# Performance work log

Hardware: AMD Instinct MI355X
Metric: run time of the kernel (lower is better)

## Reference

```python
import jax, jax.numpy as jnp
import numpy as np

T, N, E, D, NL = 2, 4096, 4096, 128, 2  # types, nodes, hyperedges, in_dim, num_layers
DENSITY = 0.002  # ~8 hyperedges per node


def setup_inputs() -> dict:
    key = jax.random.key(0)
    k1, k2, k3, k4 = jax.random.split(key, 4)
    x = jax.random.normal(k1, (N, D), dtype=jnp.float32)
    # binary incidence matrices, one per hyperedge type
    H = (jax.random.uniform(k2, (T, N, E)) < DENSITY).astype(jnp.float32)
    # nn.Linear weights (torch convention: [out, in]) and biases, per layer per type
    W = jax.random.normal(k3, (NL, T, D, D), dtype=jnp.float32) * (1.0 / np.sqrt(D))
    b = jax.random.normal(k4, (NL, T, D), dtype=jnp.float32) * 0.05
    return {"x": x, "H": H, "W": W, "b": b}


def reference(x, H, W, b):
    # degree normalizations (set_matrices): D_v^{-1/2}, D_e^{-1}, zeros kept at zero
    dV = H.sum(-1)                                  # [T,N]
    dVis = jnp.where(dV > 0, dV ** -0.5, 0.0)       # [T,N]
    dE = H.sum(1)                                   # [T,E]
    dEinv = jnp.where(dE > 0, 1.0 / dE, 0.0)        # [T,E]

    node_out = [x]
    review_out = []
    num_layers = W.shape[0]
    for l in range(num_layers):
        # per-type Linear: y = x @ W_k.T + b_k (dropout p=0 -> identity)
        xw = jnp.einsum('nd,tod->tno', x, W[l]) + b[l][:, None, :]   # [T,N,D]
        # e = L @ xw with L = Dv^{-1/2} H De^{-1} H^T Dv^{-1/2}
        y = dVis[..., None] * xw                                     # [T,N,D]
        ye = dEinv[..., None] * jnp.einsum('tne,tnd->ted', H, y)     # [T,E,D]
        e = dVis[..., None] * jnp.einsum('tne,ted->tnd', H, ye)      # [T,N,D]
        e = jax.nn.leaky_relu(e, 0.01)                               # non_linear
        # o = O @ e = De^{-1} H^T e; aggregator='sum' over types
        o = (dEinv[..., None] * jnp.einsum('tne,tnd->ted', H, e)).sum(0)  # [E,D]
        x = e.sum(0)                                                 # [N,D]
        node_out.append(x)
        review_out.append(o)

    return (jnp.stack(node_out).mean(0), jnp.stack(review_out).mean(0))
```

## Files before the change

### kernel.cpp

```cpp
#include <hip/hip_runtime.h>

#define T_ 2
#define N_ 4096
#define E_ 4096
#define D_ 128
#define CAP 64
#define PAD 16
#define SENT 8192
#define UPR 64

__device__ __forceinline__ unsigned f2bf_rne(float f) {
    unsigned u = __float_as_uint(f);
    return (u + 0x7FFFu + ((u >> 16) & 1u)) >> 16;
}
__device__ __forceinline__ unsigned pack2(float lo, float hi) {
    return f2bf_rne(lo) | (f2bf_rne(hi) << 16);
}

__device__ __forceinline__ float2 gather64(const unsigned* __restrict__ src,
        const int* __restrict__ row, int c, int lane) {
    const int4* r4 = (const int4*)row;
    int4 i0 = r4[0], i1 = r4[1], i2 = r4[2], i3 = r4[3];
    float sx = 0.f, sy = 0.f;
#define G1(id) { unsigned v = src[(size_t)(id) * UPR + lane]; \
                 sx += __uint_as_float(v << 16); \
                 sy += __uint_as_float(v & 0xFFFF0000u); }
    G1(i0.x) G1(i0.y) G1(i0.z) G1(i0.w)
    G1(i1.x) G1(i1.y) G1(i1.z) G1(i1.w)
    G1(i2.x) G1(i2.y) G1(i2.z) G1(i2.w)
    G1(i3.x) G1(i3.y) G1(i3.z) G1(i3.w)
    for (int j = PAD; j < c; ++j) G1(row[j])
#undef G1
    float2 r = {sx, sy};
    return r;
}

__device__ __forceinline__ float2 gather64w(const unsigned* __restrict__ src,
        const float* __restrict__ wgt, const int* __restrict__ row, int c, int lane) {
    const int4* r4 = (const int4*)row;
    int4 i0 = r4[0], i1 = r4[1], i2 = r4[2], i3 = r4[3];
    float sx = 0.f, sy = 0.f;
#define G1(id) { unsigned v = src[(size_t)(id) * UPR + lane]; float w = wgt[id]; \
                 sx += w * __uint_as_float(v << 16); \
                 sy += w * __uint_as_float(v & 0xFFFF0000u); }
    G1(i0.x) G1(i0.y) G1(i0.z) G1(i0.w)
    G1(i1.x) G1(i1.y) G1(i1.z) G1(i1.w)
    G1(i2.x) G1(i2.y) G1(i2.z) G1(i2.w)
    G1(i3.x) G1(i3.y) G1(i3.z) G1(i3.w)
    for (int j = PAD; j < c; ++j) G1(row[j])
#undef G1
    float2 r = {sx, sy};
    return r;
}

__device__ __forceinline__ void xw_tile(int slot, int l,
        const float* __restrict__ xsrc, const float* __restrict__ W,
        const float* __restrict__ b, uint2* __restrict__ y2,
        float* s_xs, float* s_ws) {
    int t = slot >> 7;
    int nb = (slot >> 1) & 63, ob = slot & 1;
    int n0 = nb * 64, o0 = ob * 64;
    int tid = threadIdx.x;
    int tx = tid & 15, ty = tid >> 4;
    const float* Wg = W + ((size_t)(l * T_ + t) * D_ + o0) * D_;
    const float* xg = xsrc + (size_t)n0 * D_;
    float acc[4][4] = {};
    for (int kc = 0; kc < 4; ++kc) {
        __syncthreads();
        for (int i = tid; i < 512; i += 256) {
            int r = i >> 3, k4 = i & 7;
            *(float4*)(s_xs + r * 36 + k4 * 4) =
                *(const float4*)(xg + (size_t)r * D_ + kc * 32 + k4 * 4);
            int k4s = k4 ^ ((r >> 2) & 7);
            *(float4*)(s_ws + r * 32 + k4s * 4) =
                *(const float4*)(Wg + (size_t)r * D_ + kc * 32 + k4 * 4);
        }
        __syncthreads();
        #pragma unroll
        for (int k4 = 0; k4 < 8; ++k4) {
            float4 xv[4], wv[4];
            #pragma unroll
            for (int rr = 0; rr < 4; ++rr)
                xv[rr] = *(const float4*)(s_xs + (ty * 4 + rr) * 36 + k4 * 4);
            int k4s = k4 ^ (tx & 7);
            #pragma unroll
            for (int cc = 0; cc < 4; ++cc)
                wv[cc] = *(const float4*)(s_ws + (tx * 4 + cc) * 32 + k4s * 4);
            #pragma unroll
            for (int rr = 0; rr < 4; ++rr)
                #pragma unroll
                for (int cc = 0; cc < 4; ++cc)
                    acc[rr][cc] += xv[rr].x * wv[cc].x + xv[rr].y * wv[cc].y
                                 + xv[rr].z * wv[cc].z + xv[rr].w * wv[cc].w;
        }
    }
    const float* bg = b + (size_t)(l * T_ + t) * D_;
    float4 bv = *(const float4*)(bg + o0 + tx * 4);
    #pragma unroll
    for (int rr = 0; rr < 4; ++rr) {
        int n = n0 + ty * 4 + rr;
        uint2 ov;
        ov.x = pack2(acc[rr][0] + bv.x, acc[rr][1] + bv.y);
        ov.y = pack2(acc[rr][2] + bv.z, acc[rr][3] + bv.w);
        y2[(size_t)(t * N_ + n) * (UPR / 2) + (o0 >> 2) + tx] = ov;
    }
}

__global__ __launch_bounds__(256) void k_scan_xw0(const float* __restrict__ H,
        float* __restrict__ dVis, int* __restrict__ cntNE,
        int* __restrict__ adjNE, int* __restrict__ cntENp,
        int* __restrict__ adjEN,
        const float* __restrict__ x, const float* __restrict__ W,
        const float* __restrict__ b, uint2* __restrict__ y2,
        unsigned* __restrict__ y2u, unsigned* __restrict__ ye2u,
        unsigned* __restrict__ e2u) {
    __shared__ float s_xs[64 * 36];
    __shared__ float s_ws[64 * 32];
    int bid = blockIdx.x;
    if (bid >= 2048) {
        xw_tile(bid - 2048, 0, x, W, b, y2, s_xs, s_ws);
        return;
    }
    int row = bid * 4 + (threadIdx.x >> 6);
    int lane = threadIdx.x & 63;
    int t = row >> 12;
    if (lane < PAD) adjEN[(size_t)row * CAP + lane] = SENT;
    else if (lane == PAD) cntENp[row * 16] = 0;
    if (bid == 0 && threadIdx.x < 64) {
        y2u[(size_t)SENT * UPR + threadIdx.x] = 0u;
        ye2u[(size_t)SENT * UPR + threadIdx.x] = 0u;
        e2u[(size_t)SENT * UPR + threadIdx.x] = 0u;
        if (threadIdx.x == 0) dVis[SENT] = 0.0f;
    }
    const float4* row4 = (const float4*)(H + (size_t)row * E_);
    unsigned long long mask = 0;
    #pragma unroll
    for (int i = 0; i < 16; ++i) {
        float4 v = row4[i * 64 + lane];
        unsigned mm = 0;
        if (v.x != 0.0f) mm |= 1u;
        if (v.y != 0.0f) mm |= 2u;
        if (v.z != 0.0f) mm |= 4u;
        if (v.w != 0.0f) mm |= 8u;
        mask |= (unsigned long long)mm << (i * 4);
    }
    int cnt = __popcll(mask);
    int incl = cnt;
    #pragma unroll
    for (int off = 1; off < 64; off <<= 1) {
        int u = __shfl_up(incl, off);
        if (lane >= off) incl += u;
    }
    int pos = incl - cnt;
    int total = __shfl(incl, 63);
    int* adjrow = adjNE + (size_t)row * CAP;
    unsigned long long m = mask;
    while (m) {
        int bpos = __builtin_ctzll(m);
        m &= m - 1;
        int e = ((bpos >> 2) << 8) + lane * 4 + (bpos & 3);
        if (pos < CAP) adjrow[pos] = t * E_ + e;
        ++pos;
    }
    if (lane < PAD - total) adjrow[total + lane] = SENT;
    if (lane == 63) {
        cntNE[row] = total < CAP ? total : CAP;
        dVis[row] = total > 0 ? rsqrtf((float)total) : 0.0f;
    }
}

__global__ __launch_bounds__(256) void k_inv(const int* __restrict__ cntNE,
        const int* __restrict__ adjNE, int* __restrict__ cntENp,
        int* __restrict__ adjEN) {
    int row = blockIdx.x * 4 + (threadIdx.x >> 6);
    int lane = threadIdx.x & 63;
    int c = cntNE[row];
    if (lane < c) {
        int eg = adjNE[(size_t)row * CAP + lane];
        int slot = atomicAdd(&cntENp[eg * 16], 1);
        if (slot < CAP) adjEN[(size_t)eg * CAP + slot] = row;
    }
}

__global__ __launch_bounds__(256) void k_ye_w(const unsigned* __restrict__ y2u,
        const float* __restrict__ dVis, const int* __restrict__ cntENp,
        const int* __restrict__ adjEN, unsigned* __restrict__ ye2u) {
    int u = threadIdx.x >> 6, lane = threadIdx.x & 63;
    int vr = blockIdx.x * 4 + u;
    int c = cntENp[vr * 16];
    if (c > CAP) c = CAP;
    float dE = c > 0 ? 1.0f / (float)c : 0.0f;
    float2 g = gather64w(y2u, dVis, adjEN + (size_t)vr * CAP, c, lane);
    ye2u[(size_t)vr * UPR + lane] = pack2(dE * g.x, dE * g.y);
}

__device__ __forceinline__ void o_unit(int e, int u, int lane,
        const unsigned* __restrict__ e2u, const int* __restrict__ cntENp,
        const int* __restrict__ adjEN, float2* __restrict__ revacc2,
        float2* __restrict__ outrev2, int last, float2 (*sb)[64]) {
    int t = u & 1;
    int r = t * E_ + e;
    int c = cntENp[r * 16];
    if (c > CAP) c = CAP;
    float dE = c > 0 ? 1.0f / (float)c : 0.0f;
    float2 g = gather64(e2u, adjEN + (size_t)r * CAP, c, lane);
    float2 a = {dE * g.x, dE * g.y};
    sb[u][lane] = a;
    __syncthreads();
    if (t == 0) {
        float2 o2 = sb[u | 1][lane];
        float2 tot = {a.x + o2.x, a.y + o2.y};
        size_t i = (size_t)e * UPR + lane;
        if (!last) revacc2[i] = tot;
        else {
            float2 ra = revacc2[i];
            float2 o = {(ra.x + tot.x) * 0.5f, (ra.y + tot.y) * 0.5f};
            outrev2[i] = o;
        }
    }
}

__global__ __launch_bounds__(256) void k_e(const unsigned* __restrict__ ye2u,
        const float* __restrict__ dVis, const int* __restrict__ cntNE,
        const int* __restrict__ adjNE, unsigned* __restrict__ e2u,
        const float* __restrict__ x0, float* __restrict__ xsum0,
        float* __restrict__ outnode, int last) {
    __shared__ float2 sb[4][64];
    int u = threadIdx.x >> 6, lane = threadIdx.x & 63;
    int t = u & 1;
    int n = blockIdx.x * 2 + (u >> 1);
    int r = t * N_ + n;
    int c = cntNE[r];
    float2 g = gather64(ye2u, adjNE + (size_t)r * CAP, c, lane);
    float dv = dVis[r];
    float e0 = dv * g.x; e0 = e0 >= 0.f ? e0 : 0.01f * e0;
    float e1 = dv * g.y; e1 = e1 >= 0.f ? e1 : 0.01f * e1;
    e2u[(size_t)r * UPR + lane] = pack2(e0, e1);
    float2 mine = {e0, e1};
    sb[u][lane] = mine;
    __syncthreads();
    if (t == 0) {
        float2 o2 = sb[u | 1][lane];
        float2 xnew = {e0 + o2.x, e1 + o2.y};
        size_t i = (size_t)n * UPR + lane;
        if (!last) ((float2*)xsum0)[i] = xnew;
        else {
            float2 xv = ((const float2*)x0)[i];
            float2 xs = ((const float2*)xsum0)[i];
            float2 o = {(xv.x + xs.x + xnew.x) * (1.0f / 3.0f),
                        (xv.y + xs.y + xnew.y) * (1.0f / 3.0f)};
            ((float2*)outnode)[i] = o;
        }
    }
}

__global__ __launch_bounds__(256) void k_xw1_o0(const float* __restrict__ xsum0,
        const float* __restrict__ W, const float* __restrict__ b,
        uint2* __restrict__ y2,
        const unsigned* __restrict__ e2u, const int* __restrict__ cntENp,
        const int* __restrict__ adjEN, float* __restrict__ revacc) {
    __shared__ float s_xs[64 * 36];
    __shared__ float s_ws[64 * 32];
    __shared__ float2 sb[4][64];
    int bid = blockIdx.x;
    if (bid < 256) {
        xw_tile(bid, 1, xsum0, W, b, y2, s_xs, s_ws);
    } else {
        int u = threadIdx.x >> 6, lane = threadIdx.x & 63;
        int e = (bid - 256) * 2 + (u >> 1);
        o_unit(e, u, lane, e2u, cntENp, adjEN, (float2*)revacc, nullptr, 0, sb);
    }
}

__global__ __launch_bounds__(256) void k_o(const unsigned* __restrict__ e2u,
        const int* __restrict__ cntENp, const int* __restrict__ adjEN,
        float* __restrict__ revacc, float* __restrict__ outrev) {
    __shared__ float2 sb[4][64];
    int u = threadIdx.x >> 6, lane = threadIdx.x & 63;
    int e = blockIdx.x * 2 + (u >> 1);
    o_unit(e, u, lane, e2u, cntENp, adjEN, (float2*)revacc, (float2*)outrev, 1, sb);
}

extern "C" void kernel_launch(void* const* d_in, const int* in_sizes, int n_in,
                              void* d_out, int out_size, void* d_ws, size_t ws_size,
                              hipStream_t stream) {
    const float* x = (const float*)d_in[0];
    const float* H = (const float*)d_in[1];
    const float* W = (const float*)d_in[2];
    const float* b = (const float*)d_in[3];
    float* outnode = (float*)d_out;
    float* outrev  = (float*)d_out + (size_t)N_ * D_;

    char* p = (char*)d_ws;
    auto alloc = [&](size_t bytes) {
        char* r = p;
        p += (bytes + 255) & ~(size_t)255;
        return r;
    };
    float*    dVis   = (float*)alloc(((size_t)T_ * N_ + 1) * 4);
    int*      cntNE  = (int*)  alloc((size_t)T_ * N_ * 4);
    int*      cntENp = (int*)  alloc((size_t)T_ * E_ * 16 * 4);
    int*      adjNE  = (int*)  alloc((size_t)T_ * N_ * CAP * 4);
    int*      adjEN  = (int*)  alloc((size_t)T_ * E_ * CAP * 4);
    unsigned* y2u    = (unsigned*)alloc((size_t)(SENT + 1) * UPR * 4);
    unsigned* ye2u   = (unsigned*)alloc((size_t)(SENT + 1) * UPR * 4);
    unsigned* e2u    = (unsigned*)alloc((size_t)(SENT + 1) * UPR * 4);
    float*    xsum0  = (float*)alloc((size_t)N_ * D_ * 4);
    float*    revacc = (float*)alloc((size_t)E_ * D_ * 4);

    k_scan_xw0<<<2048 + 256, 256, 0, stream>>>(H, dVis, cntNE, adjNE, cntENp,
            adjEN, x, W, b, (uint2*)y2u, y2u, ye2u, e2u);
    k_inv<<<2048, 256, 0, stream>>>(cntNE, adjNE, cntENp, adjEN);
    k_ye_w<<<2048, 256, 0, stream>>>(y2u, dVis, cntENp, adjEN, ye2u);
    k_e<<<2048, 256, 0, stream>>>(ye2u, dVis, cntNE, adjNE, e2u, x, xsum0,
                                  outnode, 0);
    k_xw1_o0<<<256 + 2048, 256, 0, stream>>>(xsum0, W, b, (uint2*)y2u,
            e2u, cntENp, adjEN, revacc);
    k_ye_w<<<2048, 256, 0, stream>>>(y2u, dVis, cntENp, adjEN, ye2u);
    k_e<<<2048, 256, 0, stream>>>(ye2u, dVis, cntNE, adjNE, e2u, x, xsum0,
                                  outnode, 1);
    k_o<<<2048, 256, 0, stream>>>(e2u, cntENp, adjEN, revacc, outrev);
}
```

Measured before the change: 86.08 us.

## Fuse hyperedge aggregation into node gather via two-hop traversal with packed weights

Removes the k_ye_w kernel and its ye2u intermediate. Each node now gathers directly over its hyperedges and then over each hyperedge's member nodes, recomputing the hyperedge sums on the fly. The node degree weight is quantised to 16 bits and packed beside the node index in the edge-to-node adjacency list, which removes a separate dVis lookup per neighbour. This saves two launches and a round trip through memory, but each hyperedge sum is recomputed once per member node, roughly eight times the gather traffic, and the 16-bit weight quantisation adds rounding error.

```diff
diff --git a/kernel.cpp b/kernel.cpp
--- a/kernel.cpp
+++ b/kernel.cpp
@@ -8,6 +8,7 @@
 #define PAD 16
 #define SENT 8192
 #define UPR 64
+#define W16S 65535.0f
 
 __device__ __forceinline__ unsigned f2bf_rne(float f) {
     unsigned u = __float_as_uint(f);
@@ -17,14 +18,14 @@
     return f2bf_rne(lo) | (f2bf_rne(hi) << 16);
 }
 
-__device__ __forceinline__ float2 gather64(const unsigned* __restrict__ src,
-        const int* __restrict__ row, int c, int lane) {
-    const int4* r4 = (const int4*)row;
-    int4 i0 = r4[0], i1 = r4[1], i2 = r4[2], i3 = r4[3];
+__device__ __forceinline__ float2 gather16_id(const unsigned* __restrict__ src,
+        const unsigned* __restrict__ row, int c, int lane) {
+    const uint4* r4 = (const uint4*)row;
+    uint4 i0 = r4[0], i1 = r4[1], i2 = r4[2], i3 = r4[3];
     float sx = 0.f, sy = 0.f;
-#define G1(id) { unsigned v = src[(size_t)(id) * UPR + lane]; \
-                 sx += __uint_as_float(v << 16); \
-                 sy += __uint_as_float(v & 0xFFFF0000u); }
+#define G1(w) { unsigned v = src[(size_t)((w) & 0xFFFFu) * UPR + lane]; \
+                sx += __uint_as_float(v << 16); \
+                sy += __uint_as_float(v & 0xFFFF0000u); }
     G1(i0.x) G1(i0.y) G1(i0.z) G1(i0.w)
     G1(i1.x) G1(i1.y) G1(i1.z) G1(i1.w)
     G1(i2.x) G1(i2.y) G1(i2.z) G1(i2.w)
@@ -35,21 +36,27 @@
     return r;
 }
 
-__device__ __forceinline__ float2 gather64w(const unsigned* __restrict__ src,
-        const float* __restrict__ wgt, const int* __restrict__ row, int c, int lane) {
-    const int4* r4 = (const int4*)row;
-    int4 i0 = r4[0], i1 = r4[1], i2 = r4[2], i3 = r4[3];
+__device__ __forceinline__ float2 inner16(int eg, int lane,
+        const unsigned* __restrict__ y2u, const int* __restrict__ cntENp,
+        const unsigned* __restrict__ adjEN) {
+    int cE = cntENp[eg * 16];
+    if (cE > CAP) cE = CAP;
+    float dE = cE > 0 ? 1.0f / (float)cE : 0.0f;
+    const unsigned* en = adjEN + (size_t)eg * CAP;
+    const uint4* r4 = (const uint4*)en;
+    uint4 i0 = r4[0], i1 = r4[1], i2 = r4[2], i3 = r4[3];
     float sx = 0.f, sy = 0.f;
-#define G1(id) { unsigned v = src[(size_t)(id) * UPR + lane]; float w = wgt[id]; \
-                 sx += w * __uint_as_float(v << 16); \
-                 sy += w * __uint_as_float(v & 0xFFFF0000u); }
+#define G1(w) { unsigned v = y2u[(size_t)((w) & 0xFFFFu) * UPR + lane]; \
+                float wt = (float)((w) >> 16) * (1.0f / W16S); \
+                sx += wt * __uint_as_float(v << 16); \
+                sy += wt * __uint_as_float(v & 0xFFFF0000u); }
     G1(i0.x) G1(i0.y) G1(i0.z) G1(i0.w)
     G1(i1.x) G1(i1.y) G1(i1.z) G1(i1.w)
     G1(i2.x) G1(i2.y) G1(i2.z) G1(i2.w)
     G1(i3.x) G1(i3.y) G1(i3.z) G1(i3.w)
-    for (int j = PAD; j < c; ++j) G1(row[j])
+    for (int j = PAD; j < cE; ++j) G1(en[j])
 #undef G1
-    float2 r = {sx, sy};
+    float2 r = {dE * sx, dE * sy};
     return r;
 }
 
@@ -109,11 +116,10 @@
 __global__ __launch_bounds__(256) void k_scan_xw0(const float* __restrict__ H,
         float* __restrict__ dVis, int* __restrict__ cntNE,
         int* __restrict__ adjNE, int* __restrict__ cntENp,
-        int* __restrict__ adjEN,
+        unsigned* __restrict__ adjEN,
         const float* __restrict__ x, const float* __restrict__ W,
         const float* __restrict__ b, uint2* __restrict__ y2,
-        unsigned* __restrict__ y2u, unsigned* __restrict__ ye2u,
-        unsigned* __restrict__ e2u) {
+        unsigned* __restrict__ y2u, unsigned* __restrict__ e2u) {
     __shared__ float s_xs[64 * 36];
     __shared__ float s_ws[64 * 32];
     int bid = blockIdx.x;
@@ -128,8 +134,9 @@
     else if (lane == PAD) cntENp[row * 16] = 0;
     if (bid == 0 && threadIdx.x < 64) {
         y2u[(size_t)SENT * UPR + threadIdx.x] = 0u;
-        ye2u[(size_t)SENT * UPR + threadIdx.x] = 0u;
         e2u[(size_t)SENT * UPR + threadIdx.x] = 0u;
+        if (threadIdx.x < PAD) adjEN[(size_t)SENT * CAP + threadIdx.x] = SENT;
+        if (threadIdx.x == PAD) cntENp[SENT * 16] = 0;
         if (threadIdx.x == 0) dVis[SENT] = 0.0f;
     }
     const float4* row4 = (const float4*)(H + (size_t)row * E_);
@@ -170,59 +177,24 @@
 }
 
 __global__ __launch_bounds__(256) void k_inv(const int* __restrict__ cntNE,
-        const int* __restrict__ adjNE, int* __restrict__ cntENp,
-        int* __restrict__ adjEN) {
+        const int* __restrict__ adjNE, const float* __restrict__ dVis,
+        int* __restrict__ cntENp, unsigned* __restrict__ adjEN) {
     int row = blockIdx.x * 4 + (threadIdx.x >> 6);
     int lane = threadIdx.x & 63;
     int c = cntNE[row];
     if (lane < c) {
         int eg = adjNE[(size_t)row * CAP + lane];
+        unsigned w16 = (unsigned)(dVis[row] * W16S + 0.5f);
         int slot = atomicAdd(&cntENp[eg * 16], 1);
-        if (slot < CAP) adjEN[(size_t)eg * CAP + slot] = row;
-    }
-}
-
-__global__ __launch_bounds__(256) void k_ye_w(const unsigned* __restrict__ y2u,
-        const float* __restrict__ dVis, const int* __restrict__ cntENp,
-        const int* __restrict__ adjEN, unsigned* __restrict__ ye2u) {
-    int u = threadIdx.x >> 6, lane = threadIdx.x & 63;
-    int vr = blockIdx.x * 4 + u;
-    int c = cntENp[vr * 16];
-    if (c > CAP) c = CAP;
-    float dE = c > 0 ? 1.0f / (float)c : 0.0f;
-    float2 g = gather64w(y2u, dVis, adjEN + (size_t)vr * CAP, c, lane);
-    ye2u[(size_t)vr * UPR + lane] = pack2(dE * g.x, dE * g.y);
-}
-
-__device__ __forceinline__ void o_unit(int e, int u, int lane,
-        const unsigned* __restrict__ e2u, const int* __restrict__ cntENp,
-        const int* __restrict__ adjEN, float2* __restrict__ revacc2,
-        float2* __restrict__ outrev2, int last, float2 (*sb)[64]) {
-    int t = u & 1;
-    int r = t * E_ + e;
-    int c = cntENp[r * 16];
-    if (c > CAP) c = CAP;
-    float dE = c > 0 ? 1.0f / (float)c : 0.0f;
-    float2 g = gather64(e2u, adjEN + (size_t)r * CAP, c, lane);
-    float2 a = {dE * g.x, dE * g.y};
-    sb[u][lane] = a;
-    __syncthreads();
-    if (t == 0) {
-        float2 o2 = sb[u | 1][lane];
-        float2 tot = {a.x + o2.x, a.y + o2.y};
-        size_t i = (size_t)e * UPR + lane;
-        if (!last) revacc2[i] = tot;
-        else {
-            float2 ra = revacc2[i];
-            float2 o = {(ra.x + tot.x) * 0.5f, (ra.y + tot.y) * 0.5f};
-            outrev2[i] = o;
-        }
-    }
-}
-
-__global__ __launch_bounds__(256) void k_e(const unsigned* __restrict__ ye2u,
+        if (slot < CAP)
+            adjEN[(size_t)eg * CAP + slot] = (unsigned)row | (w16 << 16);
+    }
+}
+
+__global__ __launch_bounds__(256) void k_e2hop(const unsigned* __restrict__ y2u,
         const float* __restrict__ dVis, const int* __restrict__ cntNE,
-        const int* __restrict__ adjNE, unsigned* __restrict__ e2u,
+        const int* __restrict__ adjNE, const int* __restrict__ cntENp,
+        const unsigned* __restrict__ adjEN, unsigned* __restrict__ e2u,
         const float* __restrict__ x0, float* __restrict__ xsum0,
         float* __restrict__ outnode, int last) {
     __shared__ float2 sb[4][64];
@@ -230,11 +202,29 @@
     int t = u & 1;
     int n = blockIdx.x * 2 + (u >> 1);
     int r = t * N_ + n;
-    int c = cntNE[r];
-    float2 g = gather64(ye2u, adjNE + (size_t)r * CAP, c, lane);
+    int cn = cntNE[r];
+    const int* an = adjNE + (size_t)r * CAP;
+    const int4* a4 = (const int4*)an;
+    float sx = 0.f, sy = 0.f;
+#define EG4(v) { \
+        float2 p0 = inner16(v.x, lane, y2u, cntENp, adjEN); \
+        float2 p1 = inner16(v.y, lane, y2u, cntENp, adjEN); \
+        float2 p2 = inner16(v.z, lane, y2u, cntENp, adjEN); \
+        float2 p3 = inner16(v.w, lane, y2u, cntENp, adjEN); \
+        sx += (p0.x + p1.x) + (p2.x + p3.x); \
+        sy += (p0.y + p1.y) + (p2.y + p3.y); }
+    if (cn > 0)  { int4 v = a4[0]; EG4(v) }
+    if (cn > 4)  { int4 v = a4[1]; EG4(v) }
+    if (cn > 8)  { int4 v = a4[2]; EG4(v) }
+    if (cn > 12) { int4 v = a4[3]; EG4(v) }
+#undef EG4
+    for (int j = PAD; j < cn; ++j) {
+        float2 p = inner16(an[j], lane, y2u, cntENp, adjEN);
+        sx += p.x; sy += p.y;
+    }
     float dv = dVis[r];
-    float e0 = dv * g.x; e0 = e0 >= 0.f ? e0 : 0.01f * e0;
-    float e1 = dv * g.y; e1 = e1 >= 0.f ? e1 : 0.01f * e1;
+    float e0 = dv * sx; e0 = e0 >= 0.f ? e0 : 0.01f * e0;
+    float e1 = dv * sy; e1 = e1 >= 0.f ? e1 : 0.01f * e1;
     e2u[(size_t)r * UPR + lane] = pack2(e0, e1);
     float2 mine = {e0, e1};
     sb[u][lane] = mine;
@@ -254,11 +244,37 @@
     }
 }
 
+__device__ __forceinline__ void o_unit(int e, int u, int lane,
+        const unsigned* __restrict__ e2u, const int* __restrict__ cntENp,
+        const unsigned* __restrict__ adjEN, float2* __restrict__ revacc2,
+        float2* __restrict__ outrev2, int last, float2 (*sb)[64]) {
+    int t = u & 1;
+    int r = t * E_ + e;
+    int c = cntENp[r * 16];
+    if (c > CAP) c = CAP;
+    float dE = c > 0 ? 1.0f / (float)c : 0.0f;
+    float2 g = gather16_id(e2u, adjEN + (size_t)r * CAP, c, lane);
+    float2 a = {dE * g.x, dE * g.y};
+    sb[u][lane] = a;
+    __syncthreads();
+    if (t == 0) {
+        float2 o2 = sb[u | 1][lane];
+        float2 tot = {a.x + o2.x, a.y + o2.y};
+        size_t i = (size_t)e * UPR + lane;
+        if (!last) revacc2[i] = tot;
+        else {
+            float2 ra = revacc2[i];
+            float2 o = {(ra.x + tot.x) * 0.5f, (ra.y + tot.y) * 0.5f};
+            outrev2[i] = o;
+        }
+    }
+}
+
 __global__ __launch_bounds__(256) void k_xw1_o0(const float* __restrict__ xsum0,
         const float* __restrict__ W, const float* __restrict__ b,
         uint2* __restrict__ y2,
         const unsigned* __restrict__ e2u, const int* __restrict__ cntENp,
-        const int* __restrict__ adjEN, float* __restrict__ revacc) {
+        const unsigned* __restrict__ adjEN, float* __restrict__ revacc) {
     __shared__ float s_xs[64 * 36];
     __shared__ float s_ws[64 * 32];
     __shared__ float2 sb[4][64];
@@ -273,7 +289,7 @@
 }
 
 __global__ __launch_bounds__(256) void k_o(const unsigned* __restrict__ e2u,
-        const int* __restrict__ cntENp, const int* __restrict__ adjEN,
+        const int* __restrict__ cntENp, const unsigned* __restrict__ adjEN,
         float* __restrict__ revacc, float* __restrict__ outrev) {
     __shared__ float2 sb[4][64];
     int u = threadIdx.x >> 6, lane = threadIdx.x & 63;
@@ -299,25 +315,22 @@
     };
     float*    dVis   = (float*)alloc(((size_t)T_ * N_ + 1) * 4);
     int*      cntNE  = (int*)  alloc((size_t)T_ * N_ * 4);
-    int*      cntENp = (int*)  alloc((size_t)T_ * E_ * 16 * 4);
+    int*      cntENp = (int*)  alloc(((size_t)T_ * E_ * 16 + 16) * 4);
     int*      adjNE  = (int*)  alloc((size_t)T_ * N_ * CAP * 4);
-    int*      adjEN  = (int*)  alloc((size_t)T_ * E_ * CAP * 4);
+    unsigned* adjEN  = (unsigned*)alloc(((size_t)T_ * E_ + 1) * CAP * 4);
     unsigned* y2u    = (unsigned*)alloc((size_t)(SENT + 1) * UPR * 4);
-    unsigned* ye2u   = (unsigned*)alloc((size_t)(SENT + 1) * UPR * 4);
     unsigned* e2u    = (unsigned*)alloc((size_t)(SENT + 1) * UPR * 4);
     float*    xsum0  = (float*)alloc((size_t)N_ * D_ * 4);
     float*    revacc = (float*)alloc((size_t)E_ * D_ * 4);
 
     k_scan_xw0<<<2048 + 256, 256, 0, stream>>>(H, dVis, cntNE, adjNE, cntENp,
-            adjEN, x, W, b, (uint2*)y2u, y2u, ye2u, e2u);
-    k_inv<<<2048, 256, 0, stream>>>(cntNE, adjNE, cntENp, adjEN);
-    k_ye_w<<<2048, 256, 0, stream>>>(y2u, dVis, cntENp, adjEN, ye2u);
-    k_e<<<2048, 256, 0, stream>>>(ye2u, dVis, cntNE, adjNE, e2u, x, xsum0,
-                                  outnode, 0);
+            adjEN, x, W, b, (uint2*)y2u, y2u, e2u);
+    k_inv<<<2048, 256, 0, stream>>>(cntNE, adjNE, dVis, cntENp, adjEN);
+    k_e2hop<<<2048, 256, 0, stream>>>(y2u, dVis, cntNE, adjNE, cntENp, adjEN,
+                                      e2u, x, xsum0, outnode, 0);
     k_xw1_o0<<<256 + 2048, 256, 0, stream>>>(xsum0, W, b, (uint2*)y2u,
             e2u, cntENp, adjEN, revacc);
-    k_ye_w<<<2048, 256, 0, stream>>>(y2u, dVis, cntENp, adjEN, ye2u);
-    k_e<<<2048, 256, 0, stream>>>(ye2u, dVis, cntNE, adjNE, e2u, x, xsum0,
-                                  outnode, 1);
+    k_e2hop<<<2048, 256, 0, stream>>>(y2u, dVis, cntNE, adjNE, cntENp, adjEN,
+                                      e2u, x, xsum0, outnode, 1);
     k_o<<<2048, 256, 0, stream>>>(e2u, cntENp, adjEN, revacc, outrev);
 }
```

New measurement: 142.1 us. +65.1%, slower.

## Build edge-to-node adjacency in scan kernel and pack node weights into indices

Applied to the files above, without the earlier changes.

The separate inversion kernel is removed. The H-scan kernel now does the atomicAdd scatter into the edge-to-node adjacency while it walks each row's set bits. Each edge-to-node entry stores the node id in the low 16 bits and a 16-bit fixed-point D_v^{-1/2} in the high bits, so the weighted gather no longer needs a dependent load from dVis. A small zero-init kernel now sets up the sentinel padding and counters before the scan. In exchange, the node weights are quantized to 16-bit fixed point, and the scan kernel takes on the atomic traffic.

```diff
diff --git a/kernel.cpp b/kernel.cpp
--- a/kernel.cpp
+++ b/kernel.cpp
@@ -8,6 +8,7 @@
 #define PAD 16
 #define SENT 8192
 #define UPR 64
+#define W16S 65535.0f
 
 __device__ __forceinline__ unsigned f2bf_rne(float f) {
     unsigned u = __float_as_uint(f);
@@ -35,14 +36,14 @@
     return r;
 }
 
-__device__ __forceinline__ float2 gather64w(const unsigned* __restrict__ src,
-        const float* __restrict__ wgt, const int* __restrict__ row, int c, int lane) {
-    const int4* r4 = (const int4*)row;
-    int4 i0 = r4[0], i1 = r4[1], i2 = r4[2], i3 = r4[3];
+__device__ __forceinline__ float2 gather16_id(const unsigned* __restrict__ src,
+        const unsigned* __restrict__ row, int c, int lane) {
+    const uint4* r4 = (const uint4*)row;
+    uint4 i0 = r4[0], i1 = r4[1], i2 = r4[2], i3 = r4[3];
     float sx = 0.f, sy = 0.f;
-#define G1(id) { unsigned v = src[(size_t)(id) * UPR + lane]; float w = wgt[id]; \
-                 sx += w * __uint_as_float(v << 16); \
-                 sy += w * __uint_as_float(v & 0xFFFF0000u); }
+#define G1(w) { unsigned v = src[(size_t)((w) & 0xFFFFu) * UPR + lane]; \
+                sx += __uint_as_float(v << 16); \
+                sy += __uint_as_float(v & 0xFFFF0000u); }
     G1(i0.x) G1(i0.y) G1(i0.z) G1(i0.w)
     G1(i1.x) G1(i1.y) G1(i1.z) G1(i1.w)
     G1(i2.x) G1(i2.y) G1(i2.z) G1(i2.w)
@@ -51,6 +52,39 @@
 #undef G1
     float2 r = {sx, sy};
     return r;
+}
+
+__device__ __forceinline__ float2 gather16_w(const unsigned* __restrict__ src,
+        const unsigned* __restrict__ row, int c, int lane) {
+    const uint4* r4 = (const uint4*)row;
+    uint4 i0 = r4[0], i1 = r4[1], i2 = r4[2], i3 = r4[3];
+    float sx = 0.f, sy = 0.f;
+#define G1(w) { unsigned v = src[(size_t)((w) & 0xFFFFu) * UPR + lane]; \
+                float wt = (float)((w) >> 16) * (1.0f / W16S); \
+                sx += wt * __uint_as_float(v << 16); \
+                sy += wt * __uint_as_float(v & 0xFFFF0000u); }
+    G1(i0.x) G1(i0.y) G1(i0.z) G1(i0.w)
+    G1(i1.x) G1(i1.y) G1(i1.z) G1(i1.w)
+    G1(i2.x) G1(i2.y) G1(i2.z) G1(i2.w)
+    G1(i3.x) G1(i3.y) G1(i3.z) G1(i3.w)
+    for (int j = PAD; j < c; ++j) G1(row[j])
+#undef G1
+    float2 r = {sx, sy};
+    return r;
+}
+
+__global__ void k_zero0(int* __restrict__ cntENp, unsigned* __restrict__ adjEN,
+                        unsigned* __restrict__ ye2u, unsigned* __restrict__ e2u) {
+    int i = blockIdx.x * 256 + threadIdx.x;
+    if (i < (T_ * E_ + 1) * PAD) {
+        int row = i >> 4, slot = i & 15;
+        adjEN[(size_t)row * CAP + slot] = SENT;
+    }
+    if (i <= T_ * E_) cntENp[i * 16] = 0;
+    if (i < 64) {
+        ye2u[(size_t)SENT * UPR + i] = 0u;
+        e2u[(size_t)SENT * UPR + i] = 0u;
+    }
 }
 
 __device__ __forceinline__ void xw_tile(int slot, int l,
@@ -106,14 +140,12 @@
     }
 }
 
-__global__ __launch_bounds__(256) void k_scan_xw0(const float* __restrict__ H,
+__global__ __launch_bounds__(256) void k_scan_inv_xw0(const float* __restrict__ H,
         float* __restrict__ dVis, int* __restrict__ cntNE,
         int* __restrict__ adjNE, int* __restrict__ cntENp,
-        int* __restrict__ adjEN,
+        unsigned* __restrict__ adjEN,
         const float* __restrict__ x, const float* __restrict__ W,
-        const float* __restrict__ b, uint2* __restrict__ y2,
-        unsigned* __restrict__ y2u, unsigned* __restrict__ ye2u,
-        unsigned* __restrict__ e2u) {
+        const float* __restrict__ b, uint2* __restrict__ y2) {
     __shared__ float s_xs[64 * 36];
     __shared__ float s_ws[64 * 32];
     int bid = blockIdx.x;
@@ -124,14 +156,6 @@
     int row = bid * 4 + (threadIdx.x >> 6);
     int lane = threadIdx.x & 63;
     int t = row >> 12;
-    if (lane < PAD) adjEN[(size_t)row * CAP + lane] = SENT;
-    else if (lane == PAD) cntENp[row * 16] = 0;
-    if (bid == 0 && threadIdx.x < 64) {
-        y2u[(size_t)SENT * UPR + threadIdx.x] = 0u;
-        ye2u[(size_t)SENT * UPR + threadIdx.x] = 0u;
-        e2u[(size_t)SENT * UPR + threadIdx.x] = 0u;
-        if (threadIdx.x == 0) dVis[SENT] = 0.0f;
-    }
     const float4* row4 = (const float4*)(H + (size_t)row * E_);
     unsigned long long mask = 0;
     #pragma unroll
@@ -153,57 +177,49 @@
     }
     int pos = incl - cnt;
     int total = __shfl(incl, 63);
+    float dv = total > 0 ? rsqrtf((float)total) : 0.0f;
+    unsigned packbase = (unsigned)row | ((unsigned)(dv * W16S + 0.5f) << 16);
     int* adjrow = adjNE + (size_t)row * CAP;
     unsigned long long m = mask;
     while (m) {
         int bpos = __builtin_ctzll(m);
         m &= m - 1;
         int e = ((bpos >> 2) << 8) + lane * 4 + (bpos & 3);
-        if (pos < CAP) adjrow[pos] = t * E_ + e;
+        int eg = t * E_ + e;
+        if (pos < CAP) adjrow[pos] = eg;
         ++pos;
+        int slot = atomicAdd(&cntENp[eg * 16], 1);
+        if (slot < CAP) adjEN[(size_t)eg * CAP + slot] = packbase;
     }
     if (lane < PAD - total) adjrow[total + lane] = SENT;
     if (lane == 63) {
         cntNE[row] = total < CAP ? total : CAP;
-        dVis[row] = total > 0 ? rsqrtf((float)total) : 0.0f;
-    }
-}
-
-__global__ __launch_bounds__(256) void k_inv(const int* __restrict__ cntNE,
-        const int* __restrict__ adjNE, int* __restrict__ cntENp,
-        int* __restrict__ adjEN) {
-    int row = blockIdx.x * 4 + (threadIdx.x >> 6);
-    int lane = threadIdx.x & 63;
-    int c = cntNE[row];
-    if (lane < c) {
-        int eg = adjNE[(size_t)row * CAP + lane];
-        int slot = atomicAdd(&cntENp[eg * 16], 1);
-        if (slot < CAP) adjEN[(size_t)eg * CAP + slot] = row;
+        dVis[row] = dv;
     }
 }
 
 __global__ __launch_bounds__(256) void k_ye_w(const unsigned* __restrict__ y2u,
-        const float* __restrict__ dVis, const int* __restrict__ cntENp,
-        const int* __restrict__ adjEN, unsigned* __restrict__ ye2u) {
+        const int* __restrict__ cntENp, const unsigned* __restrict__ adjEN,
+        unsigned* __restrict__ ye2u) {
     int u = threadIdx.x >> 6, lane = threadIdx.x & 63;
     int vr = blockIdx.x * 4 + u;
     int c = cntENp[vr * 16];
     if (c > CAP) c = CAP;
     float dE = c > 0 ? 1.0f / (float)c : 0.0f;
-    float2 g = gather64w(y2u, dVis, adjEN + (size_t)vr * CAP, c, lane);
+    float2 g = gather16_w(y2u, adjEN + (size_t)vr * CAP, c, lane);
     ye2u[(size_t)vr * UPR + lane] = pack2(dE * g.x, dE * g.y);
 }
 
 __device__ __forceinline__ void o_unit(int e, int u, int lane,
         const unsigned* __restrict__ e2u, const int* __restrict__ cntENp,
-        const int* __restrict__ adjEN, float2* __restrict__ revacc2,
+        const unsigned* __restrict__ adjEN, float2* __restrict__ revacc2,
         float2* __restrict__ outrev2, int last, float2 (*sb)[64]) {
     int t = u & 1;
     int r = t * E_ + e;
     int c = cntENp[r * 16];
     if (c > CAP) c = CAP;
     float dE = c > 0 ? 1.0f / (float)c : 0.0f;
-    float2 g = gather64(e2u, adjEN + (size_t)r * CAP, c, lane);
+    float2 g = gather16_id(e2u, adjEN + (size_t)r * CAP, c, lane);
     float2 a = {dE * g.x, dE * g.y};
     sb[u][lane] = a;
     __syncthreads();
@@ -258,7 +274,7 @@
         const float* __restrict__ W, const float* __restrict__ b,
         uint2* __restrict__ y2,
         const unsigned* __restrict__ e2u, const int* __restrict__ cntENp,
-        const int* __restrict__ adjEN, float* __restrict__ revacc) {
+        const unsigned* __restrict__ adjEN, float* __restrict__ revacc) {
     __shared__ float s_xs[64 * 36];
     __shared__ float s_ws[64 * 32];
     __shared__ float2 sb[4][64];
@@ -273,7 +289,7 @@
 }
 
 __global__ __launch_bounds__(256) void k_o(const unsigned* __restrict__ e2u,
-        const int* __restrict__ cntENp, const int* __restrict__ adjEN,
+        const int* __restrict__ cntENp, const unsigned* __restrict__ adjEN,
         float* __restrict__ revacc, float* __restrict__ outrev) {
     __shared__ float2 sb[4][64];
     int u = threadIdx.x >> 6, lane = threadIdx.x & 63;
@@ -299,24 +315,24 @@
     };
     float*    dVis   = (float*)alloc(((size_t)T_ * N_ + 1) * 4);
     int*      cntNE  = (int*)  alloc((size_t)T_ * N_ * 4);
-    int*      cntENp = (int*)  alloc((size_t)T_ * E_ * 16 * 4);
+    int*      cntENp = (int*)  alloc(((size_t)T_ * E_ + 1) * 16 * 4);
     int*      adjNE  = (int*)  alloc((size_t)T_ * N_ * CAP * 4);
-    int*      adjEN  = (int*)  alloc((size_t)T_ * E_ * CAP * 4);
+    unsigned* adjEN  = (unsigned*)alloc(((size_t)T_ * E_ + 1) * CAP * 4);
     unsigned* y2u    = (unsigned*)alloc((size_t)(SENT + 1) * UPR * 4);
     unsigned* ye2u   = (unsigned*)alloc((size_t)(SENT + 1) * UPR * 4);
     unsigned* e2u    = (unsigned*)alloc((size_t)(SENT + 1) * UPR * 4);
     float*    xsum0  = (float*)alloc((size_t)N_ * D_ * 4);
     float*    revacc = (float*)alloc((size_t)E_ * D_ * 4);
 
-    k_scan_xw0<<<2048 + 256, 256, 0, stream>>>(H, dVis, cntNE, adjNE, cntENp,
-            adjEN, x, W, b, (uint2*)y2u, y2u, ye2u, e2u);
-    k_inv<<<2048, 256, 0, stream>>>(cntNE, adjNE, cntENp, adjEN);
-    k_ye_w<<<2048, 256, 0, stream>>>(y2u, dVis, cntENp, adjEN, ye2u);
+    k_zero0<<<513, 256, 0, stream>>>(cntENp, adjEN, ye2u, e2u);
+    k_scan_inv_xw0<<<2048 + 256, 256, 0, stream>>>(H, dVis, cntNE, adjNE,
+            cntENp, adjEN, x, W, b, (uint2*)y2u);
+    k_ye_w<<<2048, 256, 0, stream>>>(y2u, cntENp, adjEN, ye2u);
     k_e<<<2048, 256, 0, stream>>>(ye2u, dVis, cntNE, adjNE, e2u, x, xsum0,
                                   outnode, 0);
     k_xw1_o0<<<256 + 2048, 256, 0, stream>>>(xsum0, W, b, (uint2*)y2u,
             e2u, cntENp, adjEN, revacc);
-    k_ye_w<<<2048, 256, 0, stream>>>(y2u, dVis, cntENp, adjEN, ye2u);
+    k_ye_w<<<2048, 256, 0, stream>>>(y2u, cntENp, adjEN, ye2u);
     k_e<<<2048, 256, 0, stream>>>(ye2u, dVis, cntNE, adjNE, e2u, x, xsum0,
                                   outnode, 1);
     k_o<<<2048, 256, 0, stream>>>(e2u, cntENp, adjEN, revacc, outrev);
```

After: 85.36 us. Within noise of the previous version (-0.8%).
